# Performance work log

Hardware: AMD Instinct MI355X
Metric: run time of the kernel (lower is better)

The kernel has to match this reference:

```python
import jax, jax.numpy as jnp
import numpy as np

N_SAMPLE = 128
POS_MAX = 32            # n_sample * pos_ratio = 128 * 0.25
POS_THR = 0.5
NEG_HI = 0.5
NEG_LO = 0.0
EPS = np.float32(np.finfo(np.float32).eps)
IMG_SIZE = 800.0


def _make_boxes(key, shape):
    # well-formed corner boxes: x1<x2, y1<y2, inside image
    k1, k2 = jax.random.split(key)
    xy = jax.random.uniform(k1, shape[:-1] + (2,)) * (IMG_SIZE - 50.0)
    wh = jax.random.uniform(k2, shape[:-1] + (2,)) * 300.0 + 1.0
    return jnp.concatenate([xy, jnp.minimum(xy + wh, IMG_SIZE)], axis=-1)


def setup_inputs() -> dict:
    key = jax.random.key(0)
    k1, k2, k3, k4 = jax.random.split(key, 4)
    roi = _make_boxes(k1, (32, 6000, 4))          # [B, R, 4]
    gt_boxes = _make_boxes(k2, (32, 100, 4))      # [B, G, 4]
    labels = jax.random.randint(k3, (32, 100), 1, 81, dtype=jnp.int32)  # [B, G]
    image = jax.random.normal(k4, (32, 3, 224, 224), dtype=jnp.float32)
    return {"roi": roi, "gt_boxes": gt_boxes, "labels": labels, "image": image}


def _iou_matrix(roi, gt):
    # roi [R,4], gt [G,4] -> [R,G]
    ix1 = jnp.maximum(roi[:, None, 0], gt[None, :, 0])
    iy1 = jnp.maximum(roi[:, None, 1], gt[None, :, 1])
    ix2 = jnp.minimum(roi[:, None, 2], gt[None, :, 2])
    iy2 = jnp.minimum(roi[:, None, 3], gt[None, :, 3])
    iw = jnp.maximum(ix2 - ix1, 0.0)
    ih = jnp.maximum(iy2 - iy1, 0.0)
    inter = iw * ih
    area_r = (roi[:, 2] - roi[:, 0]) * (roi[:, 3] - roi[:, 1])
    area_g = (gt[:, 2] - gt[:, 0]) * (gt[:, 3] - gt[:, 1])
    return inter / (area_r[:, None] + area_g[None, :] - inter)


def _rank_desc(score):
    return jnp.argsort(jnp.argsort(-score))


def _per_image(roi, gt, labels, key):
    # roi [R,4], gt [G,4], labels [G]
    ious = _iou_matrix(roi, gt)                       # [R,G]
    gt_assignment = jnp.argmax(ious, axis=1)          # [R]
    max_iou = jnp.max(ious, axis=1)                   # [R]

    pos_mask = max_iou >= POS_THR
    neg_mask = (max_iou < NEG_HI) & (max_iou >= NEG_LO)

    # random priorities emulate np.random.choice without replacement
    r = jax.random.uniform(key, (roi.shape[0],), minval=1e-6, maxval=1.0)
    pos_rank = _rank_desc(jnp.where(pos_mask, r, -1.0))
    is_sel_pos = pos_mask & (pos_rank < POS_MAX)      # min(POS_MAX, n_pos) positives
    n_pos = jnp.sum(is_sel_pos)
    neg_rank = _rank_desc(jnp.where(neg_mask, r, -1.0))
    is_sel_neg = neg_mask & (neg_rank < (N_SAMPLE - n_pos))

    # positives first (prio 2+r), then negatives (1+r), rest excluded
    prio = jnp.where(is_sel_pos, 2.0 + r, jnp.where(is_sel_neg, 1.0 + r, r - 10.0))
    vals, keep = jax.lax.top_k(prio, N_SAMPLE)        # keep [128]
    valid = vals >= 1.0
    kept_pos = is_sel_pos[keep]

    gt_roi_labels = jnp.where(kept_pos, labels[gt_assignment[keep]], 0)

    sample_roi = jnp.where(valid[:, None], roi[keep], 0.0)   # [128,4]
    base = gt[gt_assignment[keep]]                            # [128,4]

    w = jnp.maximum(roi[keep, 2] - roi[keep, 0], EPS)
    h = jnp.maximum(roi[keep, 3] - roi[keep, 1], EPS)
    cx = roi[keep, 0] + 0.5 * (roi[keep, 2] - roi[keep, 0])
    cy = roi[keep, 1] + 0.5 * (roi[keep, 3] - roi[keep, 1])
    bw = base[:, 2] - base[:, 0]
    bh = base[:, 3] - base[:, 1]
    bcx = base[:, 0] + 0.5 * bw
    bcy = base[:, 1] + 0.5 * bh

    dx = (bcx - cx) / w
    dy = (bcy - cy) / h
    dw = jnp.log(bw / w)
    dh = jnp.log(bh / h)
    deltas = jnp.where(valid[:, None], jnp.stack([dx, dy, dw, dh], axis=1), 0.0)
    return sample_roi, gt_roi_labels, deltas


def reference(roi, gt_boxes, labels, image):
    # image only used for visualization in the original; no math depends on it.
    B = roi.shape[0]
    keys = jax.random.split(jax.random.key(42), B)
    sample_roi, gt_roi_labels, gt_roi_bbox = jax.vmap(_per_image)(roi, gt_boxes, labels, keys)
    return sample_roi, gt_roi_labels, gt_roi_bbox
```

## Files before the change

### kernel.cpp

```cpp
#include <hip/hip_runtime.h>
#include <stdint.h>

#pragma clang fp contract(off)

#define B_IMG 32
#define R_N   6000
#define G_N   100
#define NS    128
#define PMAX  32
#define NBUCK 1024
#define BCAP  512
#define SEL_T 1024

#ifndef JAX_PARTITIONABLE
#define JAX_PARTITIONABLE 1
#endif

__device__ __forceinline__ uint32_t rotl32(uint32_t v, int d) {
  return (v << d) | (v >> (32 - d));
}

__device__ __forceinline__ void tf2x32(uint32_t k0, uint32_t k1,
                                       uint32_t x0, uint32_t x1,
                                       uint32_t& o0, uint32_t& o1) {
  const uint32_t k2 = k0 ^ k1 ^ 0x1BD11BDAu;
  x0 += k0; x1 += k1;
#define TF_R(r) { x0 += x1; x1 = rotl32(x1, r); x1 ^= x0; }
  TF_R(13) TF_R(15) TF_R(26) TF_R(6)
  x0 += k1; x1 += k2 + 1u;
  TF_R(17) TF_R(29) TF_R(16) TF_R(24)
  x0 += k2; x1 += k0 + 2u;
  TF_R(13) TF_R(15) TF_R(26) TF_R(6)
  x0 += k0; x1 += k1 + 3u;
  TF_R(17) TF_R(29) TF_R(16) TF_R(24)
  x0 += k1; x1 += k2 + 4u;
  TF_R(13) TF_R(15) TF_R(26) TF_R(6)
  x0 += k2; x1 += k0 + 5u;
#undef TF_R
  o0 = x0; o1 = x1;
}

__device__ __forceinline__ float tf_uniform(uint32_t bits) {
#pragma clang fp contract(off)
  float f = __uint_as_float((bits >> 9) | 0x3f800000u) - 1.0f;
  float r = f * (1.0f - 1e-6f) + 1e-6f;
  return fmaxf(1e-6f, r);
}

__global__ __launch_bounds__(256) void prep_kernel(
    const float* __restrict__ roi, const float* __restrict__ gt,
    float* __restrict__ wr, float* __restrict__ wmiou, int* __restrict__ wgta) {
#pragma clang fp contract(off)
  const int b = blockIdx.y;
  const int i = blockIdx.x * 256 + threadIdx.x;

  __shared__ float sg[G_N * 4];
  __shared__ float sga[G_N];
  for (int t = threadIdx.x; t < G_N * 4; t += 256) sg[t] = gt[b * G_N * 4 + t];
  __syncthreads();
  if (threadIdx.x < G_N) {
    int g = threadIdx.x;
    sga[g] = (sg[g * 4 + 2] - sg[g * 4 + 0]) * (sg[g * 4 + 3] - sg[g * 4 + 1]);
  }
  __syncthreads();
  if (i >= R_N) return;

  const float* rp = roi + ((size_t)b * R_N + i) * 4;
  float x1 = rp[0], y1 = rp[1], x2 = rp[2], y2 = rp[3];
  float ar = (x2 - x1) * (y2 - y1);

  float best = -1.0f; int bi = 0;
  for (int g = 0; g < G_N; ++g) {
    float gx1 = sg[g * 4 + 0], gy1 = sg[g * 4 + 1];
    float gx2 = sg[g * 4 + 2], gy2 = sg[g * 4 + 3];
    float ix1 = fmaxf(x1, gx1), iy1 = fmaxf(y1, gy1);
    float ix2 = fminf(x2, gx2), iy2 = fminf(y2, gy2);
    float iw = fmaxf(ix2 - ix1, 0.0f);
    float ih = fmaxf(iy2 - iy1, 0.0f);
    float inter = iw * ih;
    float denom = (ar + sga[g]) - inter;
    float iou = inter / denom;
    if (iou > best) { best = iou; bi = g; }
  }

  uint32_t bits;
#if JAX_PARTITIONABLE
  uint32_t kb0, kb1;
  tf2x32(0u, 42u, 0u, (uint32_t)b, kb0, kb1);
  uint32_t t0, t1;
  tf2x32(kb0, kb1, 0u, (uint32_t)i, t0, t1);
  bits = t0 ^ t1;
#else
  uint32_t kb0, kb1, d0, d1;
  if (b < 16) {
    tf2x32(0u, 42u, (uint32_t)(2 * b),     (uint32_t)(2 * b + 32), kb0, d0);
    tf2x32(0u, 42u, (uint32_t)(2 * b + 1), (uint32_t)(2 * b + 33), kb1, d1);
  } else {
    int c = b - 16;
    tf2x32(0u, 42u, (uint32_t)(2 * c),     (uint32_t)(2 * c + 32), d0, kb0);
    tf2x32(0u, 42u, (uint32_t)(2 * c + 1), (uint32_t)(2 * c + 33), d1, kb1);
  }
  uint32_t t0, t1;
  if (i < R_N / 2) { tf2x32(kb0, kb1, (uint32_t)i, (uint32_t)(i + R_N / 2), t0, t1); bits = t0; }
  else             { tf2x32(kb0, kb1, (uint32_t)(i - R_N / 2), (uint32_t)i, t0, t1); bits = t1; }
#endif

  size_t o = (size_t)b * R_N + i;
  wr[o] = tf_uniform(bits);
  wmiou[o] = best;
  wgta[o] = bi;
}

__global__ __launch_bounds__(SEL_T) void select_kernel(
    const float* __restrict__ roi, const float* __restrict__ gt,
    const int* __restrict__ labels,
    const float* __restrict__ wr, const float* __restrict__ wmiou,
    const int* __restrict__ wgta, float* __restrict__ out) {
#pragma clang fp contract(off)
  const int b = blockIdx.x;
  const int tid = threadIdx.x;

  __shared__ float sr[R_N];
  __shared__ unsigned char scls[R_N];
  __shared__ unsigned char ssel[R_N];
  __shared__ int S[NBUCK];
  __shared__ int sh_cntpos;
  __shared__ int sh_B, sh_A;
  __shared__ int candIdx[BCAP];
  __shared__ int candCnt;
  __shared__ int posList[PMAX];
  __shared__ int negList[NS];
  __shared__ int listCnt[2];
  __shared__ int outIdx[NS];

  if (tid == 0) sh_cntpos = 0;
  if (tid < 2) listCnt[tid] = 0;
  __syncthreads();

  int mycnt = 0;
  for (int i = tid; i < R_N; i += SEL_T) {
    sr[i] = wr[(size_t)b * R_N + i];
    unsigned char p = (wmiou[(size_t)b * R_N + i] >= 0.5f) ? 1 : 0;
    scls[i] = p;
    ssel[i] = 0;
    mycnt += p;
  }
  if (mycnt) atomicAdd(&sh_cntpos, mycnt);
  __syncthreads();

  const int cntPos = sh_cntpos;
  const int cntNeg = R_N - cntPos;
  const int nPosSel = min(cntPos, PMAX);
  const int Kneg = NS - nPosSel;

  for (int c = 1; c >= 0; --c) {
    const int quota = (c == 1) ? PMAX : Kneg;
    const int cnt   = (c == 1) ? cntPos : cntNeg;
    if (cnt <= quota) {
      for (int i = tid; i < R_N; i += SEL_T)
        if (scls[i] == (unsigned char)c) ssel[i] = 1;
      __syncthreads();
      continue;
    }
    if (tid < NBUCK) S[tid] = 0;
    if (tid == 0) candCnt = 0;
    __syncthreads();
    for (int i = tid; i < R_N; i += SEL_T)
      if (scls[i] == (unsigned char)c) {
        int bk = min((int)(sr[i] * (float)NBUCK), NBUCK - 1);
        atomicAdd(&S[bk], 1);
      }
    __syncthreads();
    for (int off = 1; off < NBUCK; off <<= 1) {
      int v = 0;
      if (tid < NBUCK && tid + off < NBUCK) v = S[tid + off];
      __syncthreads();
      if (tid < NBUCK) S[tid] += v;
      __syncthreads();
    }
    if (tid < NBUCK) {
      int Sh = S[tid];
      int Sn = (tid + 1 < NBUCK) ? S[tid + 1] : 0;
      if (Sh >= quota && Sn < quota) { sh_B = tid; sh_A = Sn; }
    }
    __syncthreads();
    const int Bb = sh_B, A = sh_A;
    for (int i = tid; i < R_N; i += SEL_T)
      if (scls[i] == (unsigned char)c) {
        int bk = min((int)(sr[i] * (float)NBUCK), NBUCK - 1);
        if (bk > Bb) ssel[i] = 1;
        else if (bk == Bb) {
          int p = atomicAdd(&candCnt, 1);
          if (p < BCAP) candIdx[p] = i;
        }
      }
    __syncthreads();
    const int M = candCnt;
    if (M <= BCAP) {
      if (tid < M) {
        int i = candIdx[tid];
        float ri = sr[i];
        int beats = 0;
        for (int u = 0; u < M; ++u) {
          int j = candIdx[u];
          float rj = sr[j];
          if (rj > ri || (rj == ri && j < i)) beats++;
        }
        if (A + beats < quota) ssel[i] = 1;
      }
    } else {
      for (int i = tid; i < R_N; i += SEL_T)
        if (scls[i] == (unsigned char)c) {
          int bk = min((int)(sr[i] * (float)NBUCK), NBUCK - 1);
          if (bk == Bb) {
            float ri = sr[i];
            int beats = 0;
            for (int j = 0; j < R_N; ++j)
              if (scls[j] == (unsigned char)c) {
                float rj = sr[j];
                int bj = min((int)(rj * (float)NBUCK), NBUCK - 1);
                if (bj == Bb && (rj > ri || (rj == ri && j < i))) beats++;
              }
            if (A + beats < quota) ssel[i] = 1;
          }
        }
    }
    __syncthreads();
  }

  for (int i = tid; i < R_N; i += SEL_T)
    if (ssel[i]) {
      if (scls[i]) { int p = atomicAdd(&listCnt[1], 1); if (p < PMAX) posList[p] = i; }
      else         { int p = atomicAdd(&listCnt[0], 1); if (p < NS)   negList[p] = i; }
    }
  __syncthreads();
  const int nP = min(listCnt[1], PMAX);
  const int nN = min(listCnt[0], NS);

  if (tid < NS) outIdx[tid] = -1;
  __syncthreads();

  if (tid < nP) {
    int i = posList[tid];
    float pr = 2.0f + sr[i];
    int slot = 0;
    for (int u = 0; u < nP; ++u) {
      int j = posList[u];
      float pj = 2.0f + sr[j];
      if (pj > pr || (pj == pr && j < i)) slot++;
    }
    outIdx[slot] = i;
  }
  if (tid < nN) {
    int i = negList[tid];
    float pr = 1.0f + sr[i];
    int slot = 0;
    for (int u = 0; u < nN; ++u) {
      int j = negList[u];
      float pj = 1.0f + sr[j];
      if (pj > pr || (pj == pr && j < i)) slot++;
    }
    outIdx[nP + slot] = i;
  }
  __syncthreads();

  if (tid < NS) {
    const int p = tid;
    const int i = outIdx[p];
    float o_roi[4] = {0.f, 0.f, 0.f, 0.f};
    float o_lab = 0.f;
    float o_d[4] = {0.f, 0.f, 0.f, 0.f};
    if (i >= 0) {
      const float* rp = roi + ((size_t)b * R_N + i) * 4;
      float x1 = rp[0], y1 = rp[1], x2 = rp[2], y2 = rp[3];
      o_roi[0] = x1; o_roi[1] = y1; o_roi[2] = x2; o_roi[3] = y2;
      int g = wgta[(size_t)b * R_N + i];
      const float* gp = gt + ((size_t)b * G_N + g) * 4;
      float gx1 = gp[0], gy1 = gp[1], gx2 = gp[2], gy2 = gp[3];
      if (scls[i]) o_lab = (float)labels[b * G_N + g];
      const float EPSF = 1.1920928955078125e-7f;
      float w = fmaxf(x2 - x1, EPSF);
      float h = fmaxf(y2 - y1, EPSF);
      float cx = x1 + 0.5f * (x2 - x1);
      float cy = y1 + 0.5f * (y2 - y1);
      float bw = gx2 - gx1, bh = gy2 - gy1;
      float bcx = gx1 + 0.5f * bw, bcy = gy1 + 0.5f * bh;
      o_d[0] = (bcx - cx) / w;
      o_d[1] = (bcy - cy) / h;
      o_d[2] = logf(bw / w);
      o_d[3] = logf(bh / h);
    }
    float* out0 = out;
    float* out1 = out + (size_t)B_IMG * NS * 4;
    float* out2 = out1 + (size_t)B_IMG * NS;
    const int base = b * NS + p;
    out0[base * 4 + 0] = o_roi[0];
    out0[base * 4 + 1] = o_roi[1];
    out0[base * 4 + 2] = o_roi[2];
    out0[base * 4 + 3] = o_roi[3];
    out1[base] = o_lab;
    out2[base * 4 + 0] = o_d[0];
    out2[base * 4 + 1] = o_d[1];
    out2[base * 4 + 2] = o_d[2];
    out2[base * 4 + 3] = o_d[3];
  }
}

extern "C" void kernel_launch(void* const* d_in, const int* in_sizes, int n_in,
                              void* d_out, int out_size, void* d_ws, size_t ws_size,
                              hipStream_t stream) {
  const float* roi    = (const float*)d_in[0];
  const float* gt     = (const float*)d_in[1];
  const int*   labels = (const int*)d_in[2];

  float* wr    = (float*)d_ws;
  float* wmiou = wr + (size_t)B_IMG * R_N;
  int*   wgta  = (int*)(wmiou + (size_t)B_IMG * R_N);

  dim3 g1((R_N + 255) / 256, B_IMG);
  prep_kernel<<<g1, 256, 0, stream>>>(roi, gt, wr, wmiou, wgta);
  select_kernel<<<B_IMG, SEL_T, 0, stream>>>(roi, gt, labels, wr, wmiou, wgta,
                                             (float*)d_out);
}
```

Measured before the change: 107.4 us.

## Keep per-thread ROI scores in registers and use wavefront-shuffle scans in selection

New measurement: 109.6 us. 1.02x slower.

```diff
diff --git a/kernel.cpp b/kernel.cpp
--- a/kernel.cpp
+++ b/kernel.cpp
@@ -11,6 +11,7 @@
 #define NBUCK 1024
 #define BCAP  512
 #define SEL_T 1024
+#define KPT   6
 
 #ifndef JAX_PARTITIONABLE
 #define JAX_PARTITIONABLE 1
@@ -47,6 +48,10 @@
   return fmaxf(1e-6f, r);
 }
 
+__device__ __forceinline__ int bucket_of(float r) {
+  return min((int)(r * (float)NBUCK), NBUCK - 1);
+}
+
 __global__ __launch_bounds__(256) void prep_kernel(
     const float* __restrict__ roi, const float* __restrict__ gt,
     float* __restrict__ wr, float* __restrict__ wmiou, int* __restrict__ wgta) {
@@ -65,8 +70,8 @@
   __syncthreads();
   if (i >= R_N) return;
 
-  const float* rp = roi + ((size_t)b * R_N + i) * 4;
-  float x1 = rp[0], y1 = rp[1], x2 = rp[2], y2 = rp[3];
+  const float4 rv = ((const float4*)roi)[(size_t)b * R_N + i];
+  float x1 = rv.x, y1 = rv.y, x2 = rv.z, y2 = rv.w;
   float ar = (x2 - x1) * (y2 - y1);
 
   float best = -1.0f; int bi = 0;
@@ -119,33 +124,39 @@
 #pragma clang fp contract(off)
   const int b = blockIdx.x;
   const int tid = threadIdx.x;
-
-  __shared__ float sr[R_N];
-  __shared__ unsigned char scls[R_N];
-  __shared__ unsigned char ssel[R_N];
-  __shared__ int S[NBUCK];
-  __shared__ int sh_cntpos;
-  __shared__ int sh_B, sh_A;
-  __shared__ int candIdx[BCAP];
-  __shared__ int candCnt;
-  __shared__ int posList[PMAX];
-  __shared__ int negList[NS];
-  __shared__ int listCnt[2];
-  __shared__ int outIdx[NS];
-
-  if (tid == 0) sh_cntpos = 0;
-  if (tid < 2) listCnt[tid] = 0;
-  __syncthreads();
-
+  const int lane = tid & 63;
+  const int wid = tid >> 6;
+
+  __shared__ int   S[NBUCK];
+  __shared__ int   wsum[16];
+  __shared__ int   sh_cntpos;
+  __shared__ int   sh_B, sh_A;
+  __shared__ int   candIdx[BCAP];
+  __shared__ float candR[BCAP];
+  __shared__ int   candCnt;
+  __shared__ int   posIdx[PMAX];
+  __shared__ float posR[PMAX];
+  __shared__ int   negIdx[NS];
+  __shared__ float negR[NS];
+  __shared__ int   listCnt[2];
+  __shared__ int   outIdx[NS];
+
+  if (tid == 0) { sh_cntpos = 0; listCnt[0] = 0; listCnt[1] = 0; }
+  if (tid < NS) outIdx[tid] = -1;
+
+  float r[KPT];
+  unsigned char cls[KPT];
   int mycnt = 0;
-  for (int i = tid; i < R_N; i += SEL_T) {
-    sr[i] = wr[(size_t)b * R_N + i];
-    unsigned char p = (wmiou[(size_t)b * R_N + i] >= 0.5f) ? 1 : 0;
-    scls[i] = p;
-    ssel[i] = 0;
-    mycnt += p;
-  }
-  if (mycnt) atomicAdd(&sh_cntpos, mycnt);
+  for (int k = 0; k < KPT; ++k) {
+    int i = tid + k * SEL_T;
+    if (i < R_N) {
+      r[k] = wr[(size_t)b * R_N + i];
+      cls[k] = (wmiou[(size_t)b * R_N + i] >= 0.5f) ? 1 : 0;
+      mycnt += cls[k];
+    } else { r[k] = -1.0f; cls[k] = 255; }
+  }
+  for (int d = 32; d > 0; d >>= 1) mycnt += __shfl_down(mycnt, d);
+  if (lane == 0 && mycnt) atomicAdd(&sh_cntpos, mycnt);
   __syncthreads();
 
   const int cntPos = sh_cntpos;
@@ -156,108 +167,126 @@
   for (int c = 1; c >= 0; --c) {
     const int quota = (c == 1) ? PMAX : Kneg;
     const int cnt   = (c == 1) ? cntPos : cntNeg;
+    int*   lidx = (c == 1) ? posIdx : negIdx;
+    float* lr   = (c == 1) ? posR   : negR;
+    const int cap = (c == 1) ? PMAX : NS;
+
     if (cnt <= quota) {
-      for (int i = tid; i < R_N; i += SEL_T)
-        if (scls[i] == (unsigned char)c) ssel[i] = 1;
+      for (int k = 0; k < KPT; ++k)
+        if (cls[k] == (unsigned char)c) {
+          int p = atomicAdd(&listCnt[c], 1);
+          if (p < cap) { lidx[p] = tid + k * SEL_T; lr[p] = r[k]; }
+        }
       __syncthreads();
       continue;
     }
-    if (tid < NBUCK) S[tid] = 0;
+
+    S[tid] = 0;
     if (tid == 0) candCnt = 0;
     __syncthreads();
-    for (int i = tid; i < R_N; i += SEL_T)
-      if (scls[i] == (unsigned char)c) {
-        int bk = min((int)(sr[i] * (float)NBUCK), NBUCK - 1);
-        atomicAdd(&S[bk], 1);
+    for (int k = 0; k < KPT; ++k)
+      if (cls[k] == (unsigned char)c) atomicAdd(&S[bucket_of(r[k])], 1);
+    __syncthreads();
+
+    int v = S[NBUCK - 1 - tid];
+    for (int d = 1; d < 64; d <<= 1) {
+      int n = __shfl_up(v, d);
+      if (lane >= d) v += n;
+    }
+    if (lane == 63) wsum[wid] = v;
+    __syncthreads();
+    if (wid == 0) {
+      int t = (lane < 16) ? wsum[lane] : 0;
+      for (int d = 1; d < 16; d <<= 1) {
+        int n = __shfl_up(t, d);
+        if (lane >= d) t += n;
       }
-    __syncthreads();
-    for (int off = 1; off < NBUCK; off <<= 1) {
-      int v = 0;
-      if (tid < NBUCK && tid + off < NBUCK) v = S[tid + off];
-      __syncthreads();
-      if (tid < NBUCK) S[tid] += v;
-      __syncthreads();
-    }
-    if (tid < NBUCK) {
+      if (lane < 16) wsum[lane] = t;
+    }
+    __syncthreads();
+    int Sval = v + ((wid > 0) ? wsum[wid - 1] : 0);
+    S[NBUCK - 1 - tid] = Sval;
+    __syncthreads();
+
+    {
       int Sh = S[tid];
       int Sn = (tid + 1 < NBUCK) ? S[tid + 1] : 0;
       if (Sh >= quota && Sn < quota) { sh_B = tid; sh_A = Sn; }
     }
     __syncthreads();
     const int Bb = sh_B, A = sh_A;
-    for (int i = tid; i < R_N; i += SEL_T)
-      if (scls[i] == (unsigned char)c) {
-        int bk = min((int)(sr[i] * (float)NBUCK), NBUCK - 1);
-        if (bk > Bb) ssel[i] = 1;
-        else if (bk == Bb) {
+
+    for (int k = 0; k < KPT; ++k)
+      if (cls[k] == (unsigned char)c) {
+        int bk = bucket_of(r[k]);
+        if (bk > Bb) {
+          int p = atomicAdd(&listCnt[c], 1);
+          if (p < cap) { lidx[p] = tid + k * SEL_T; lr[p] = r[k]; }
+        } else if (bk == Bb) {
           int p = atomicAdd(&candCnt, 1);
-          if (p < BCAP) candIdx[p] = i;
+          if (p < BCAP) { candIdx[p] = tid + k * SEL_T; candR[p] = r[k]; }
         }
       }
     __syncthreads();
+
     const int M = candCnt;
     if (M <= BCAP) {
       if (tid < M) {
         int i = candIdx[tid];
-        float ri = sr[i];
+        float ri = candR[tid];
         int beats = 0;
         for (int u = 0; u < M; ++u) {
           int j = candIdx[u];
-          float rj = sr[j];
+          float rj = candR[u];
           if (rj > ri || (rj == ri && j < i)) beats++;
         }
-        if (A + beats < quota) ssel[i] = 1;
+        if (A + beats < quota) {
+          int p = atomicAdd(&listCnt[c], 1);
+          if (p < cap) { lidx[p] = i; lr[p] = ri; }
+        }
       }
     } else {
-      for (int i = tid; i < R_N; i += SEL_T)
-        if (scls[i] == (unsigned char)c) {
-          int bk = min((int)(sr[i] * (float)NBUCK), NBUCK - 1);
-          if (bk == Bb) {
-            float ri = sr[i];
-            int beats = 0;
-            for (int j = 0; j < R_N; ++j)
-              if (scls[j] == (unsigned char)c) {
-                float rj = sr[j];
-                int bj = min((int)(rj * (float)NBUCK), NBUCK - 1);
-                if (bj == Bb && (rj > ri || (rj == ri && j < i))) beats++;
-              }
-            if (A + beats < quota) ssel[i] = 1;
+      for (int k = 0; k < KPT; ++k)
+        if (cls[k] == (unsigned char)c && bucket_of(r[k]) == Bb) {
+          int i = tid + k * SEL_T;
+          float ri = r[k];
+          int beats = 0;
+          for (int j = 0; j < R_N; ++j) {
+            float rj = wr[(size_t)b * R_N + j];
+            unsigned char cj = (wmiou[(size_t)b * R_N + j] >= 0.5f) ? 1 : 0;
+            if (cj == (unsigned char)c && bucket_of(rj) == Bb &&
+                (rj > ri || (rj == ri && j < i))) beats++;
           }
-        }
-    }
-    __syncthreads();
-  }
-
-  for (int i = tid; i < R_N; i += SEL_T)
-    if (ssel[i]) {
-      if (scls[i]) { int p = atomicAdd(&listCnt[1], 1); if (p < PMAX) posList[p] = i; }
-      else         { int p = atomicAdd(&listCnt[0], 1); if (p < NS)   negList[p] = i; }
-    }
-  __syncthreads();
+          if (A + beats < quota) {
+            int p = atomicAdd(&listCnt[c], 1);
+            if (p < cap) { lidx[p] = i; lr[p] = ri; }
+          }
+        }
+    }
+    __syncthreads();
+  }
+
   const int nP = min(listCnt[1], PMAX);
   const int nN = min(listCnt[0], NS);
 
-  if (tid < NS) outIdx[tid] = -1;
-  __syncthreads();
-
   if (tid < nP) {
-    int i = posList[tid];
-    float pr = 2.0f + sr[i];
+    int i = posIdx[tid];
+    float pr = 2.0f + posR[tid];
     int slot = 0;
     for (int u = 0; u < nP; ++u) {
-      int j = posList[u];
-      float pj = 2.0f + sr[j];
+      int j = posIdx[u];
+      float pj = 2.0f + posR[u];
       if (pj > pr || (pj == pr && j < i)) slot++;
     }
     outIdx[slot] = i;
   }
   if (tid < nN) {
-    int i = negList[tid];
-    float pr = 1.0f + sr[i];
+    int i = negIdx[tid];
+    float pr = 1.0f + negR[tid];
     int slot = 0;
     for (int u = 0; u < nN; ++u) {
-      int j = negList[u];
-      float pj = 1.0f + sr[j];
+      int j = negIdx[u];
+      float pj = 1.0f + negR[u];
       if (pj > pr || (pj == pr && j < i)) slot++;
     }
     outIdx[nP + slot] = i;
@@ -271,13 +300,13 @@
     float o_lab = 0.f;
     float o_d[4] = {0.f, 0.f, 0.f, 0.f};
     if (i >= 0) {
-      const float* rp = roi + ((size_t)b * R_N + i) * 4;
-      float x1 = rp[0], y1 = rp[1], x2 = rp[2], y2 = rp[3];
+      const float4 rv = ((const float4*)roi)[(size_t)b * R_N + i];
+      float x1 = rv.x, y1 = rv.y, x2 = rv.z, y2 = rv.w;
       o_roi[0] = x1; o_roi[1] = y1; o_roi[2] = x2; o_roi[3] = y2;
       int g = wgta[(size_t)b * R_N + i];
-      const float* gp = gt + ((size_t)b * G_N + g) * 4;
-      float gx1 = gp[0], gy1 = gp[1], gx2 = gp[2], gy2 = gp[3];
-      if (scls[i]) o_lab = (float)labels[b * G_N + g];
+      const float4 gv = ((const float4*)gt)[(size_t)b * G_N + g];
+      float gx1 = gv.x, gy1 = gv.y, gx2 = gv.z, gy2 = gv.w;
+      if (p < nP) o_lab = (float)labels[b * G_N + g];
       const float EPSF = 1.1920928955078125e-7f;
       float w = fmaxf(x2 - x1, EPSF);
       float h = fmaxf(y2 - y1, EPSF);
```
